# Performance work log

Hardware: AMD Instinct MI355X
Metric: run time of the kernel (lower is better)

Reference implementation:

```python
import jax, jax.numpy as jnp
import numpy as np

BETA = 0.02
TOPK = 5  # torch.topk(A, k=5) is hard-coded; forward arg k is ignored


def setup_inputs() -> dict:
    key = jax.random.key(0)
    k1, k2, k3 = jax.random.split(key, 3)
    B, Cx, C1, CA, N, D, L = 4, 16, 16, 8, 1024, 64, 64
    x = jax.random.normal(k1, (B, Cx, N, D), dtype=jnp.float32)
    A = jax.random.normal(k2, (B, CA, N, N), dtype=jnp.float32)
    mask = jax.random.uniform(k3, (B, C1, N, L), dtype=jnp.float32)
    return {"x": x, "A": A, "mask": mask, "k": 5}


def reference(x, A, mask, k):
    # x: (B,Cx,N,D), A: (B,CA,N,N), mask: (B,C1,N,L)
    # S = softmax(x @ x^T) over last dim, then mean over channel dim -> (B,1,N,N)
    S = jax.nn.softmax(jnp.einsum('bcnd,bcmd->bcnm', x, x), axis=-1)
    S = jnp.mean(S, axis=1, keepdims=True)
    # mask similarity: (B,C1,N,N)
    mm = jnp.einsum('bcnl,bcml->bcnm', mask, mask)
    mask_weight = jax.nn.sigmoid(S * mm / jnp.sqrt(jnp.float32(10.0)))
    # A averaged over its channel dim, broadcast-added -> (B,C1,N,N)
    A_out = jnp.mean(A, axis=1, keepdims=True) + BETA * mask_weight
    # top-5 neighbors per row, gather their mask rows, reduce with max
    _, idx = jax.lax.top_k(A_out, TOPK)              # (B,C1,N,5) int32
    # mask_select[b,c,i,j,l] = mask[b,c,idx[b,c,i,j],l]
    gather = jax.vmap(jax.vmap(lambda m, i: m[i]))(mask, idx)  # (B,C1,N,5,L)
    mask_updated = jnp.max(gather, axis=-2)          # (B,C1,N,L)
    return A_out, mask_updated
```

## Files before the change

kernel.cpp:

```cpp
#include <hip/hip_runtime.h>
#include <math.h>

#define NB 4
#define NCX 16
#define NC1 16
#define NCA 8
#define NN 1024
#define ND 64
#define NL 64
#define LSTRIDE 1028
#define NCG 4

typedef __attribute__((ext_vector_type(8))) short bf16x8;
typedef __attribute__((ext_vector_type(4))) float f32x4;
typedef unsigned short u16;
typedef unsigned int u32;

__device__ __forceinline__ u16 f2b(float f) {
    u32 u = __float_as_uint(f);
    return (u16)((u + 0x7FFFu + ((u >> 16) & 1u)) >> 16);
}

__device__ __forceinline__ bf16x8 cvt8(const float* __restrict__ p) {
    float4 a = *(const float4*)p;
    float4 b = *(const float4*)(p + 4);
    bf16x8 r;
    r[0] = (short)f2b(a.x); r[1] = (short)f2b(a.y);
    r[2] = (short)f2b(a.z); r[3] = (short)f2b(a.w);
    r[4] = (short)f2b(b.x); r[5] = (short)f2b(b.y);
    r[6] = (short)f2b(b.z); r[7] = (short)f2b(b.w);
    return r;
}

__device__ __forceinline__ float sigm(float z) {
    return 1.0f / (1.0f + __expf(-z));
}

__global__ __launch_bounds__(256) void k_cvt(const float* __restrict__ src,
                                             u16* __restrict__ dst) {
    int id = blockIdx.x * 256 + threadIdx.x;
    const float4* x4 = (const float4*)src;
    float4 a = x4[2 * id];
    float4 b = x4[2 * id + 1];
    union { u16 u[8]; uint4 v; } o;
    o.u[0] = f2b(a.x); o.u[1] = f2b(a.y); o.u[2] = f2b(a.z); o.u[3] = f2b(a.w);
    o.u[4] = f2b(b.x); o.u[5] = f2b(b.y); o.u[6] = f2b(b.z); o.u[7] = f2b(b.w);
    ((uint4*)dst)[id] = o.v;
}

__global__ __launch_bounds__(256) void k_meanA(const float* __restrict__ A,
                                               float* __restrict__ meanA) {
    int id = blockIdx.x * 256 + threadIdx.x;
    int b  = id >> 18;
    int e  = id & 262143;
    const float4* A4 = (const float4*)A;
    float4 s = A4[(size_t)(b * NCA) * 262144 + e];
#pragma unroll
    for (int c = 1; c < NCA; ++c) {
        float4 v = A4[(size_t)(b * NCA + c) * 262144 + e];
        s.x += v.x; s.y += v.y; s.z += v.z; s.w += v.w;
    }
    s.x *= 0.125f; s.y *= 0.125f; s.z *= 0.125f; s.w *= 0.125f;
    ((float4*)meanA)[id] = s;
}

__global__ __launch_bounds__(1024, 8) void k_smean4(const u16* __restrict__ xb,
                                                    float* __restrict__ Spart) {
    __shared__ float L[16 * LSTRIDE];
    const int t  = threadIdx.x;
    const int w  = t >> 6;
    const int l  = t & 63;
    const int lm = l & 15;
    const int lq = l >> 4;
    const int i0 = blockIdx.x * 16;
    const int b  = blockIdx.y;
    const int cg = blockIdx.z;
    const int rb = lq * 4;

    float mean[16];
#pragma unroll
    for (int u = 0; u < 16; ++u) mean[u] = 0.f;

    const int arow = i0 + lm;

    for (int c = cg * 4; c < cg * 4 + 4; ++c) {
        const u16* Xc = xb + (size_t)(b * NCX + c) * NN * ND;
        bf16x8 a0 = *(const bf16x8*)(Xc + arow * ND + lq * 8);
        bf16x8 a1 = *(const bf16x8*)(Xc + arow * ND + 32 + lq * 8);
#pragma unroll
        for (int tt = 0; tt < 4; ++tt) {
            int j0 = w * 64 + tt * 16;
            const u16* Bp = Xc + (j0 + lm) * ND;
            bf16x8 b0 = *(const bf16x8*)(Bp + lq * 8);
            bf16x8 b1 = *(const bf16x8*)(Bp + 32 + lq * 8);
            f32x4 acc = {0.f, 0.f, 0.f, 0.f};
            acc = __builtin_amdgcn_mfma_f32_16x16x32_bf16(a0, b0, acc, 0, 0, 0);
            acc = __builtin_amdgcn_mfma_f32_16x16x32_bf16(a1, b1, acc, 0, 0, 0);
            int col = j0 + lm;
            L[(rb + 0) * LSTRIDE + col] = acc[0];
            L[(rb + 1) * LSTRIDE + col] = acc[1];
            L[(rb + 2) * LSTRIDE + col] = acc[2];
            L[(rb + 3) * LSTRIDE + col] = acc[3];
        }
        __syncthreads();
        {
            const float* Lp = &L[w * LSTRIDE];
            float v[16];
#pragma unroll
            for (int u = 0; u < 4; ++u) {
                float4 q = *(const float4*)&Lp[4 * l + 256 * u];
                v[4 * u + 0] = q.x; v[4 * u + 1] = q.y;
                v[4 * u + 2] = q.z; v[4 * u + 3] = q.w;
            }
            float m = v[0];
#pragma unroll
            for (int u = 1; u < 16; ++u) m = fmaxf(m, v[u]);
#pragma unroll
            for (int off = 32; off; off >>= 1) m = fmaxf(m, __shfl_xor(m, off, 64));
            float sum = 0.f;
#pragma unroll
            for (int u = 0; u < 16; ++u) { v[u] = __expf(v[u] - m); sum += v[u]; }
#pragma unroll
            for (int off = 32; off; off >>= 1) sum += __shfl_xor(sum, off, 64);
            float r = 1.0f / sum;
#pragma unroll
            for (int u = 0; u < 16; ++u) mean[u] = fmaf(v[u], r, mean[u]);
        }
        __syncthreads();
    }
    float* Sp = Spart + (((size_t)(cg * NB + b)) * NN + (i0 + w)) * NN;
#pragma unroll
    for (int u = 0; u < 4; ++u) {
        float4 o;
        o.x = mean[4 * u + 0]; o.y = mean[4 * u + 1];
        o.z = mean[4 * u + 2]; o.w = mean[4 * u + 3];
        *(float4*)(Sp + 4 * l + 256 * u) = o;
    }
}

__global__ __launch_bounds__(256) void k_sred(const float* __restrict__ Spart,
                                              float* __restrict__ Smean) {
    int id = blockIdx.x * 256 + threadIdx.x;
    int b  = id >> 18;
    int e  = id & 262143;
    const float4* P4 = (const float4*)Spart;
    float4 s = P4[(size_t)b * 262144 + e];
#pragma unroll
    for (int g = 1; g < NCG; ++g) {
        float4 v = P4[(size_t)(g * NB + b) * 262144 + e];
        s.x += v.x; s.y += v.y; s.z += v.z; s.w += v.w;
    }
    s.x *= 0.0625f; s.y *= 0.0625f; s.z *= 0.0625f; s.w *= 0.0625f;
    ((float4*)Smean)[id] = s;
}

template <bool MB>
__global__ __launch_bounds__(1024, 8) void k_final4(const float* __restrict__ mask,
                                                    const u16* __restrict__ maskb,
                                                    const float* __restrict__ Smean,
                                                    const float* __restrict__ meanA,
                                                    float* __restrict__ Aout,
                                                    float* __restrict__ maskUpd) {
    __shared__ float L[16 * LSTRIDE];
    const int t  = threadIdx.x;
    const int w  = t >> 6;
    const int l  = t & 63;
    const int lm = l & 15;
    const int lq = l >> 4;
    const int i0 = blockIdx.x * 16;
    const int c1 = blockIdx.y;
    const int b  = blockIdx.z;
    const int rb = lq * 4;
    const int row = i0 + w;

    const float* mbase = mask + (size_t)(b * NC1 + c1) * NN * NL;
    const u16*   mbb   = maskb + (size_t)(b * NC1 + c1) * NN * NL;

    bf16x8 a0, a1;
    if (MB) {
        a0 = *(const bf16x8*)(mbb + (i0 + lm) * NL + lq * 8);
        a1 = *(const bf16x8*)(mbb + (i0 + lm) * NL + 32 + lq * 8);
    } else {
        a0 = cvt8(mbase + (i0 + lm) * NL + lq * 8);
        a1 = cvt8(mbase + (i0 + lm) * NL + 32 + lq * 8);
    }
#pragma unroll
    for (int tt = 0; tt < 4; ++tt) {
        int j0 = w * 64 + tt * 16;
        bf16x8 b0, b1;
        if (MB) {
            const u16* Bp = mbb + (j0 + lm) * NL;
            b0 = *(const bf16x8*)(Bp + lq * 8);
            b1 = *(const bf16x8*)(Bp + 32 + lq * 8);
        } else {
            const float* Bp = mbase + (j0 + lm) * NL;
            b0 = cvt8(Bp + lq * 8);
            b1 = cvt8(Bp + 32 + lq * 8);
        }
        f32x4 acc = {0.f, 0.f, 0.f, 0.f};
        acc = __builtin_amdgcn_mfma_f32_16x16x32_bf16(a0, b0, acc, 0, 0, 0);
        acc = __builtin_amdgcn_mfma_f32_16x16x32_bf16(a1, b1, acc, 0, 0, 0);
        int col = j0 + lm;
        L[(rb + 0) * LSTRIDE + col] = acc[0];
        L[(rb + 1) * LSTRIDE + col] = acc[1];
        L[(rb + 2) * LSTRIDE + col] = acc[2];
        L[(rb + 3) * LSTRIDE + col] = acc[3];
    }

    const float* Sp = Smean + ((size_t)b * NN + row) * NN;
    float4 S4r[4];
#pragma unroll
    for (int u = 0; u < 4; ++u) S4r[u] = *(const float4*)(Sp + 4 * l + 256 * u);

    __syncthreads();

    const float* Lp = &L[w * LSTRIDE];
    const float* Mp = meanA + ((size_t)b * NN + row) * NN;
    float* Ap = Aout + ((size_t)(b * NC1 + c1) * NN + row) * NN;

    float lg[16];
#pragma unroll
    for (int u = 0; u < 4; ++u) {
        int j = 4 * l + 256 * u;
        float4 mm4 = *(const float4*)&Lp[j];
        float4 S4  = S4r[u];
        float4 M4  = *(const float4*)(Mp + j);
        float4 o;
        o.x = M4.x + 0.02f * sigm(S4.x * mm4.x * 0.31622776601683794f);
        o.y = M4.y + 0.02f * sigm(S4.y * mm4.y * 0.31622776601683794f);
        o.z = M4.z + 0.02f * sigm(S4.z * mm4.z * 0.31622776601683794f);
        o.w = M4.w + 0.02f * sigm(S4.w * mm4.w * 0.31622776601683794f);
        *(float4*)(Ap + j) = o;
        lg[4 * u + 0] = o.x; lg[4 * u + 1] = o.y;
        lg[4 * u + 2] = o.z; lg[4 * u + 3] = o.w;
    }

    int idxs[5];
#pragma unroll
    for (int p = 0; p < 5; ++p) {
        float bv = lg[0];
        int   bj = 4 * l;
#pragma unroll
        for (int k = 1; k < 16; ++k) {
            int j = 4 * l + 256 * (k >> 2) + (k & 3);
            if (lg[k] > bv) { bv = lg[k]; bj = j; }
        }
#pragma unroll
        for (int off = 32; off; off >>= 1) {
            float ov = __shfl_xor(bv, off, 64);
            int   oj = __shfl_xor(bj, off, 64);
            if (ov > bv || (ov == bv && oj < bj)) { bv = ov; bj = oj; }
        }
        idxs[p] = bj;
        const bool mine = ((bj & 255) >> 2) == l;
        const int  ck   = (bj >> 8) * 4 + (bj & 3);
#pragma unroll
        for (int k = 0; k < 16; ++k)
            lg[k] = (mine && k == ck) ? -INFINITY : lg[k];
    }
    float mx = mbase[(size_t)idxs[0] * NL + l];
#pragma unroll
    for (int p = 1; p < 5; ++p)
        mx = fmaxf(mx, mbase[(size_t)idxs[p] * NL + l]);
    maskUpd[((size_t)(b * NC1 + c1) * NN + row) * NL + l] = mx;
}

extern "C" void kernel_launch(void* const* d_in, const int* in_sizes, int n_in,
                              void* d_out, int out_size, void* d_ws, size_t ws_size,
                              hipStream_t stream) {
    const float* x    = (const float*)d_in[0];
    const float* A    = (const float*)d_in[1];
    const float* mask = (const float*)d_in[2];
    float* out     = (float*)d_out;
    float* Aout    = out;
    float* maskUpd = out + (size_t)NB * NC1 * NN * NN;
    float* meanA   = (float*)d_ws;
    float* Smean   = meanA + (size_t)NB * NN * NN;
    u16*   maskb   = (u16*)(Smean + (size_t)NB * NN * NN);
    const bool useMB = ws_size >= (size_t)(2 * NB * NN * NN * 4 + NB * NC1 * NN * NL * 2);

    u16*   xb    = (u16*)Aout;
    float* Spart = Aout + (size_t)16777216;

    hipLaunchKernelGGL(k_cvt, dim3((NB * NCX * NN * ND / 8) / 256), dim3(256), 0,
                       stream, x, xb);
    if (useMB)
        hipLaunchKernelGGL(k_cvt, dim3((NB * NC1 * NN * NL / 8) / 256), dim3(256), 0,
                           stream, mask, (u16*)maskb);
    hipLaunchKernelGGL(k_meanA, dim3((NB * NN * NN / 4) / 256), dim3(256), 0, stream,
                       A, meanA);
    hipLaunchKernelGGL(k_smean4, dim3(NN / 16, NB, NCG), dim3(1024), 0, stream,
                       xb, Spart);
    hipLaunchKernelGGL(k_sred, dim3((NB * NN * NN / 4) / 256), dim3(256), 0, stream,
                       Spart, Smean);
    if (useMB)
        hipLaunchKernelGGL(k_final4<true>, dim3(NN / 16, NC1, NB), dim3(1024), 0,
                           stream, mask, maskb, Smean, meanA, Aout, maskUpd);
    else
        hipLaunchKernelGGL(k_final4<false>, dim3(NN / 16, NC1, NB), dim3(1024), 0,
                           stream, mask, maskb, Smean, meanA, Aout, maskUpd);
}
```

Before: 593.4 us.

## Shrink row tiles to 8 with 512-thread blocks and fp16 LDS staging

```diff
diff --git a/kernel.cpp b/kernel.cpp
--- a/kernel.cpp
+++ b/kernel.cpp
@@ -8,11 +8,12 @@
 #define NN 1024
 #define ND 64
 #define NL 64
-#define LSTRIDE 1028
 #define NCG 4
+#define HSTRIDE 1028
 
 typedef __attribute__((ext_vector_type(8))) short bf16x8;
 typedef __attribute__((ext_vector_type(4))) float f32x4;
+typedef _Float16 h4 __attribute__((ext_vector_type(4)));
 typedef unsigned short u16;
 typedef unsigned int u32;
 
@@ -64,15 +65,15 @@
     ((float4*)meanA)[id] = s;
 }
 
-__global__ __launch_bounds__(1024, 8) void k_smean4(const u16* __restrict__ xb,
-                                                    float* __restrict__ Spart) {
-    __shared__ float L[16 * LSTRIDE];
+__global__ __launch_bounds__(512, 8) void k_smean5(const u16* __restrict__ xb,
+                                                   float* __restrict__ Spart) {
+    __shared__ _Float16 Lh[8 * HSTRIDE];
     const int t  = threadIdx.x;
     const int w  = t >> 6;
     const int l  = t & 63;
     const int lm = l & 15;
     const int lq = l >> 4;
-    const int i0 = blockIdx.x * 16;
+    const int i0 = blockIdx.x * 8;
     const int b  = blockIdx.y;
     const int cg = blockIdx.z;
     const int rb = lq * 4;
@@ -81,36 +82,38 @@
 #pragma unroll
     for (int u = 0; u < 16; ++u) mean[u] = 0.f;
 
-    const int arow = i0 + lm;
+    const int arow = min(i0 + lm, NN - 1);
 
     for (int c = cg * 4; c < cg * 4 + 4; ++c) {
         const u16* Xc = xb + (size_t)(b * NCX + c) * NN * ND;
         bf16x8 a0 = *(const bf16x8*)(Xc + arow * ND + lq * 8);
         bf16x8 a1 = *(const bf16x8*)(Xc + arow * ND + 32 + lq * 8);
 #pragma unroll
-        for (int tt = 0; tt < 4; ++tt) {
-            int j0 = w * 64 + tt * 16;
+        for (int tt = 0; tt < 8; ++tt) {
+            int j0 = w * 128 + tt * 16;
             const u16* Bp = Xc + (j0 + lm) * ND;
             bf16x8 b0 = *(const bf16x8*)(Bp + lq * 8);
             bf16x8 b1 = *(const bf16x8*)(Bp + 32 + lq * 8);
             f32x4 acc = {0.f, 0.f, 0.f, 0.f};
             acc = __builtin_amdgcn_mfma_f32_16x16x32_bf16(a0, b0, acc, 0, 0, 0);
             acc = __builtin_amdgcn_mfma_f32_16x16x32_bf16(a1, b1, acc, 0, 0, 0);
-            int col = j0 + lm;
-            L[(rb + 0) * LSTRIDE + col] = acc[0];
-            L[(rb + 1) * LSTRIDE + col] = acc[1];
-            L[(rb + 2) * LSTRIDE + col] = acc[2];
-            L[(rb + 3) * LSTRIDE + col] = acc[3];
+            if (lq < 2) {
+                int col = j0 + lm;
+                Lh[(rb + 0) * HSTRIDE + col] = (_Float16)acc[0];
+                Lh[(rb + 1) * HSTRIDE + col] = (_Float16)acc[1];
+                Lh[(rb + 2) * HSTRIDE + col] = (_Float16)acc[2];
+                Lh[(rb + 3) * HSTRIDE + col] = (_Float16)acc[3];
+            }
         }
         __syncthreads();
         {
-            const float* Lp = &L[w * LSTRIDE];
+            const _Float16* Lp = &Lh[w * HSTRIDE];
             float v[16];
 #pragma unroll
             for (int u = 0; u < 4; ++u) {
-                float4 q = *(const float4*)&Lp[4 * l + 256 * u];
-                v[4 * u + 0] = q.x; v[4 * u + 1] = q.y;
-                v[4 * u + 2] = q.z; v[4 * u + 3] = q.w;
+                h4 q = *(const h4*)&Lp[4 * l + 256 * u];
+                v[4 * u + 0] = (float)q[0]; v[4 * u + 1] = (float)q[1];
+                v[4 * u + 2] = (float)q[2]; v[4 * u + 3] = (float)q[3];
             }
             float m = v[0];
 #pragma unroll
@@ -155,19 +158,19 @@
 }
 
 template <bool MB>
-__global__ __launch_bounds__(1024, 8) void k_final4(const float* __restrict__ mask,
-                                                    const u16* __restrict__ maskb,
-                                                    const float* __restrict__ Smean,
-                                                    const float* __restrict__ meanA,
-                                                    float* __restrict__ Aout,
-                                                    float* __restrict__ maskUpd) {
-    __shared__ float L[16 * LSTRIDE];
+__global__ __launch_bounds__(512, 8) void k_final5(const float* __restrict__ mask,
+                                                   const u16* __restrict__ maskb,
+                                                   const float* __restrict__ Smean,
+                                                   const float* __restrict__ meanA,
+                                                   float* __restrict__ Aout,
+                                                   float* __restrict__ maskUpd) {
+    __shared__ _Float16 Lh[8 * HSTRIDE];
     const int t  = threadIdx.x;
     const int w  = t >> 6;
     const int l  = t & 63;
     const int lm = l & 15;
     const int lq = l >> 4;
-    const int i0 = blockIdx.x * 16;
+    const int i0 = blockIdx.x * 8;
     const int c1 = blockIdx.y;
     const int b  = blockIdx.z;
     const int rb = lq * 4;
@@ -176,17 +179,18 @@
     const float* mbase = mask + (size_t)(b * NC1 + c1) * NN * NL;
     const u16*   mbb   = maskb + (size_t)(b * NC1 + c1) * NN * NL;
 
+    const int arow = min(i0 + lm, NN - 1);
     bf16x8 a0, a1;
     if (MB) {
-        a0 = *(const bf16x8*)(mbb + (i0 + lm) * NL + lq * 8);
-        a1 = *(const bf16x8*)(mbb + (i0 + lm) * NL + 32 + lq * 8);
+        a0 = *(const bf16x8*)(mbb + arow * NL + lq * 8);
+        a1 = *(const bf16x8*)(mbb + arow * NL + 32 + lq * 8);
     } else {
-        a0 = cvt8(mbase + (i0 + lm) * NL + lq * 8);
-        a1 = cvt8(mbase + (i0 + lm) * NL + 32 + lq * 8);
-    }
-#pragma unroll
-    for (int tt = 0; tt < 4; ++tt) {
-        int j0 = w * 64 + tt * 16;
+        a0 = cvt8(mbase + arow * NL + lq * 8);
+        a1 = cvt8(mbase + arow * NL + 32 + lq * 8);
+    }
+#pragma unroll
+    for (int tt = 0; tt < 8; ++tt) {
+        int j0 = w * 128 + tt * 16;
         bf16x8 b0, b1;
         if (MB) {
             const u16* Bp = mbb + (j0 + lm) * NL;
@@ -200,21 +204,18 @@
         f32x4 acc = {0.f, 0.f, 0.f, 0.f};
         acc = __builtin_amdgcn_mfma_f32_16x16x32_bf16(a0, b0, acc, 0, 0, 0);
         acc = __builtin_amdgcn_mfma_f32_16x16x32_bf16(a1, b1, acc, 0, 0, 0);
-        int col = j0 + lm;
-        L[(rb + 0) * LSTRIDE + col] = acc[0];
-        L[(rb + 1) * LSTRIDE + col] = acc[1];
-        L[(rb + 2) * LSTRIDE + col] = acc[2];
-        L[(rb + 3) * LSTRIDE + col] = acc[3];
-    }
-
+        if (lq < 2) {
+            int col = j0 + lm;
+            Lh[(rb + 0) * HSTRIDE + col] = (_Float16)acc[0];
+            Lh[(rb + 1) * HSTRIDE + col] = (_Float16)acc[1];
+            Lh[(rb + 2) * HSTRIDE + col] = (_Float16)acc[2];
+            Lh[(rb + 3) * HSTRIDE + col] = (_Float16)acc[3];
+        }
+    }
+    __syncthreads();
+
+    const _Float16* Lp = &Lh[w * HSTRIDE];
     const float* Sp = Smean + ((size_t)b * NN + row) * NN;
-    float4 S4r[4];
-#pragma unroll
-    for (int u = 0; u < 4; ++u) S4r[u] = *(const float4*)(Sp + 4 * l + 256 * u);
-
-    __syncthreads();
-
-    const float* Lp = &L[w * LSTRIDE];
     const float* Mp = meanA + ((size_t)b * NN + row) * NN;
     float* Ap = Aout + ((size_t)(b * NC1 + c1) * NN + row) * NN;
 
@@ -222,14 +223,14 @@
 #pragma unroll
     for (int u = 0; u < 4; ++u) {
         int j = 4 * l + 256 * u;
-        float4 mm4 = *(const float4*)&Lp[j];
-        float4 S4  = S4r[u];
-        float4 M4  = *(const float4*)(Mp + j);
+        h4 q = *(const h4*)&Lp[j];
+        float4 S4 = *(const float4*)(Sp + j);
+        float4 M4 = *(const float4*)(Mp + j);
         float4 o;
-        o.x = M4.x + 0.02f * sigm(S4.x * mm4.x * 0.31622776601683794f);
-        o.y = M4.y + 0.02f * sigm(S4.y * mm4.y * 0.31622776601683794f);
-        o.z = M4.z + 0.02f * sigm(S4.z * mm4.z * 0.31622776601683794f);
-        o.w = M4.w + 0.02f * sigm(S4.w * mm4.w * 0.31622776601683794f);
+        o.x = M4.x + 0.02f * sigm(S4.x * (float)q[0] * 0.31622776601683794f);
+        o.y = M4.y + 0.02f * sigm(S4.y * (float)q[1] * 0.31622776601683794f);
+        o.z = M4.z + 0.02f * sigm(S4.z * (float)q[2] * 0.31622776601683794f);
+        o.w = M4.w + 0.02f * sigm(S4.w * (float)q[3] * 0.31622776601683794f);
         *(float4*)(Ap + j) = o;
         lg[4 * u + 0] = o.x; lg[4 * u + 1] = o.y;
         lg[4 * u + 2] = o.z; lg[4 * u + 3] = o.w;
@@ -289,14 +290,14 @@
                            stream, mask, (u16*)maskb);
     hipLaunchKernelGGL(k_meanA, dim3((NB * NN * NN / 4) / 256), dim3(256), 0, stream,
                        A, meanA);
-    hipLaunchKernelGGL(k_smean4, dim3(NN / 16, NB, NCG), dim3(1024), 0, stream,
+    hipLaunchKernelGGL(k_smean5, dim3(NN / 8, NB, NCG), dim3(512), 0, stream,
                        xb, Spart);
     hipLaunchKernelGGL(k_sred, dim3((NB * NN * NN / 4) / 256), dim3(256), 0, stream,
                        Spart, Smean);
     if (useMB)
-        hipLaunchKernelGGL(k_final4<true>, dim3(NN / 16, NC1, NB), dim3(1024), 0,
+        hipLaunchKernelGGL(k_final5<true>, dim3(NN / 8, NC1, NB), dim3(512), 0,
                            stream, mask, maskb, Smean, meanA, Aout, maskUpd);
     else
-        hipLaunchKernelGGL(k_final4<false>, dim3(NN / 16, NC1, NB), dim3(1024), 0,
+        hipLaunchKernelGGL(k_final5<false>, dim3(NN / 8, NC1, NB), dim3(512), 0,
                            stream, mask, maskb, Smean, meanA, Aout, maskUpd);
 }
```

Result: slower. 679.4 us (+14.5%).
